# Performance work log

Hardware: AMD Instinct MI355X
Metric: run time of the kernel (lower is better)

Reference implementation:

```python
import jax, jax.numpy as jnp
import numpy as np

T, N, E = 12, 20000, 320000
FIN, H, G, C = 128, 256, 256, 10


def setup_inputs() -> dict:
    key = jax.random.key(0)
    ks = jax.random.split(key, 14)
    x = jax.random.normal(ks[0], (T, N, FIN), dtype=jnp.float32)
    edge_index = jax.random.randint(ks[1], (T, 2, E), 0, N)
    edge_attr = jax.random.uniform(ks[2], (T, E), dtype=jnp.float32)

    def lin(k, fan_in, shape):
        return jax.random.normal(k, shape, dtype=jnp.float32) / np.sqrt(fan_in).astype(np.float32)

    return {
        "x": x,
        "edge_index": edge_index,
        "edge_attr": edge_attr,
        "W1": lin(ks[3], FIN, (FIN, H)),
        "b1": jnp.zeros((H,), jnp.float32),
        "W2": lin(ks[4], H, (H, H)),
        "b2": jnp.zeros((H,), jnp.float32),
        "Wih": lin(ks[5], H, (3 * G, H)),
        "Whh": lin(ks[6], G, (3 * G, G)),
        "bih": jnp.zeros((3 * G,), jnp.float32),
        "bhh": jnp.zeros((3 * G,), jnp.float32),
        "Wc": lin(ks[7], G, (G, C)),
        "bc": jnp.zeros((C,), jnp.float32),
    }


def _gcn_conv(h, row, col, w, W, b):
    # PyG GCNConv: h' = D^{-1/2} (A + I) D^{-1/2} (h W) + b, with edge weights w
    h = h @ W  # [N, H]
    deg = jax.ops.segment_sum(w, col, num_segments=N) + 1.0  # self-loop weight 1
    dinv = jax.lax.rsqrt(deg)  # [N]
    norm = dinv[row] * w * dinv[col]  # [E]
    agg = jax.ops.segment_sum(norm[:, None] * h[row], col, num_segments=N)
    agg = agg + (dinv * dinv)[:, None] * h  # self-loop contribution
    return agg + b


def reference(x, edge_index, edge_attr, W1, b1, W2, b2, Wih, Whh, bih, bhh, Wc, bc):
    def snapshot(carry, inp):
        xs, ei, ea = inp
        row, col = ei[0], ei[1]
        h = jax.nn.relu(_gcn_conv(xs, row, col, ea, W1, b1))
        h = jax.nn.relu(_gcn_conv(h, row, col, ea, W2, b2))
        return carry, h.mean(axis=0)  # mean pool over nodes -> [H]

    _, embs = jax.lax.scan(snapshot, 0, (x, edge_index, edge_attr))  # [T, H]

    def gru_step(hprev, xt):
        gx = Wih @ xt + bih  # [3G]
        gh = Whh @ hprev + bhh
        r = jax.nn.sigmoid(gx[:G] + gh[:G])
        z = jax.nn.sigmoid(gx[G:2 * G] + gh[G:2 * G])
        n = jnp.tanh(gx[2 * G:] + r * gh[2 * G:])
        hnew = (1.0 - z) * n + z * hprev
        return hnew, None

    last_h, _ = jax.lax.scan(gru_step, jnp.zeros((G,), x.dtype), embs)
    out = last_h @ Wc + bc  # [C]
    return out[None, :]  # [1, num_classes]
```

## Files before the change

kernel.cpp:

```cpp
#include <hip/hip_runtime.h>
#include <hip/hip_fp16.h>
#include <math.h>

#define T_ 12
#define N_ 20000
#define E_ 320000
#define FIN_ 128
#define H_ 256
#define G_ 256
#define C_ 10
#define ECH 8
#define EPC (E_ / ECH)
#define NB 20
#define BNODES 1024
#define CAPF 20480

typedef __attribute__((ext_vector_type(8))) short bf16x8;
typedef __attribute__((ext_vector_type(4))) float f32x4;

static const size_t OFF_EMB   = 0;
static const size_t ZERO_BYTES= 12288;
static const size_t OFF_DINV  = 12288;
static const size_t OFF_CP    = 972288;
static const size_t OFF_PCNT  = 1932544;
static const size_t OFF_POFF  = 1940224;
static const size_t OFF_W1BT  = 1948288;
static const size_t OFF_W2BT  = 2013824;
static const size_t OFF_WIHT  = 2144896;
static const size_t OFF_WHHT  = 2931328;
static const size_t OFF_GX    = 3717760;
static const size_t OFF_EBIN  = 3754752;
static const size_t OFF_DEGP  = 3754752;
static const size_t OFF_CNT16 = 11434752;
static const size_t OFF_RA    = 34474752;
static const size_t PER_T_FULL= 10240000;

__device__ __forceinline__ float bf2f(unsigned short u) {
  return __uint_as_float(((unsigned int)u) << 16);
}
__device__ __forceinline__ unsigned short f2bf(float f) {
  unsigned int u = __float_as_uint(f);
  unsigned int r = (u + 0x7FFFu + ((u >> 16) & 1u)) >> 16;
  return (unsigned short)r;
}
__device__ __forceinline__ float bflo(unsigned int u) { return __uint_as_float(u << 16); }
__device__ __forceinline__ float bfhi(unsigned int u) { return __uint_as_float(u & 0xFFFF0000u); }
__device__ __forceinline__ unsigned int packbf(float lo, float hi) {
  return (unsigned int)f2bf(lo) | ((unsigned int)f2bf(hi) << 16);
}

__global__ __launch_bounds__(1024) void histp(const int* __restrict__ ei,
                                              const float* __restrict__ ea,
                                              float* __restrict__ degp,
                                              unsigned short* __restrict__ cnt16,
                                              unsigned int* __restrict__ pcnt) {
  __shared__ float degs[N_];
  __shared__ unsigned int cntp[N_ / 2];
  __shared__ unsigned int psum[NB];
  const int t = blockIdx.x, ech = blockIdx.y;
  const int tid = threadIdx.x;
  for (int i = tid; i < N_; i += 1024) degs[i] = 0.f;
  for (int i = tid; i < N_ / 2; i += 1024) cntp[i] = 0u;
  if (tid < NB) psum[tid] = 0u;
  __syncthreads();
  const int* col = ei + (size_t)t * 2 * E_ + E_ + ech * EPC;
  const float* wt = ea + (size_t)t * E_ + ech * EPC;
  for (int e = tid; e < EPC; e += 1024) {
    int c = col[e];
    atomicAdd(&degs[c], wt[e]);
    atomicAdd(&cntp[c >> 1], 1u << ((c & 1) * 16));
  }
  __syncthreads();
  float* dp = degp + ((size_t)t * ECH + ech) * N_;
  unsigned short* cp16 = cnt16 + ((size_t)t * ECH + ech) * N_;
  for (int i = tid; i < N_; i += 1024) {
    dp[i] = degs[i];
    cp16[i] = (unsigned short)((cntp[i >> 1] >> ((i & 1) * 16)) & 0xFFFFu);
  }
  for (int i = tid; i < N_ / 2; i += 1024) {
    unsigned int v = cntp[i];
    atomicAdd(&psum[i >> 9], (v & 0xFFFFu) + (v >> 16));
  }
  __syncthreads();
  if (tid < NB) pcnt[((size_t)t * ECH + ech) * NB + tid] = psum[tid];
}

__global__ __launch_bounds__(1024) void scanT(const unsigned short* __restrict__ cnt16,
                                              const float* __restrict__ degp,
                                              int* __restrict__ colptr,
                                              float* __restrict__ dinv) {
  const int t = blockIdx.x;
  __shared__ int s[1024];
  const int tid = threadIdx.x;
  int base = 0;
  for (int c0 = 0; c0 < N_; c0 += 1024) {
    int n = c0 + tid;
    int tot = 0;
    float dg = 0.f;
    if (n < N_) {
#pragma unroll
      for (int ch = 0; ch < ECH; ++ch) {
        tot += cnt16[((size_t)t * ECH + ch) * N_ + n];
        dg += degp[((size_t)t * ECH + ch) * N_ + n];
      }
    }
    s[tid] = tot;
    __syncthreads();
    for (int off = 1; off < 1024; off <<= 1) {
      int add = (tid >= off) ? s[tid - off] : 0;
      __syncthreads();
      s[tid] += add;
      __syncthreads();
    }
    if (n < N_) {
      colptr[t * (N_ + 1) + n] = base + s[tid] - tot;
      dinv[t * N_ + n] = rsqrtf(dg + 1.0f);
    }
    base += s[1023];
    __syncthreads();
  }
  if (tid == 0) colptr[t * (N_ + 1) + N_] = base;
}

__global__ void partS(const unsigned int* __restrict__ pcnt,
                      unsigned int* __restrict__ poff) {
  const int t = threadIdx.x;
  if (t >= T_) return;
  unsigned int run = 0;
  for (int b = 0; b < NB; ++b)
    for (int ech = 0; ech < ECH; ++ech) {
      poff[t * 168 + b * 8 + ech] = run;
      run += pcnt[((size_t)t * ECH + ech) * NB + b];
    }
  poff[t * 168 + 160] = run;
}

__global__ __launch_bounds__(512) void partW(const int* __restrict__ ei,
                                             const float* __restrict__ ea,
                                             const float* __restrict__ dinv,
                                             const unsigned int* __restrict__ poff,
                                             uint2* __restrict__ ebin) {
  __shared__ unsigned int cursor[NB];
  const int t = blockIdx.x, ech = blockIdx.y;
  const int tid = threadIdx.x;
  if (tid < NB) cursor[tid] = poff[t * 168 + tid * 8 + ech];
  __syncthreads();
  const int eoff = ech * EPC;
  const int* rowp = ei + (size_t)t * 2 * E_ + eoff;
  const int* colp = rowp + E_;
  const float* wt = ea + (size_t)t * E_ + eoff;
  const float* dv = dinv + (size_t)t * N_;
  uint2* eb = ebin + (size_t)t * E_;
  for (int e = tid; e < EPC; e += 512) {
    int c = colp[e], r = rowp[e];
    float nm = dv[r] * wt[e] * dv[c];
    unsigned int pos = atomicAdd(&cursor[c >> 10], 1u);
    uint2 rec;
    rec.x = (unsigned int)(c & 1023) | ((unsigned int)r << 16);
    rec.y = (unsigned int)__half_as_ushort(__float2half(nm));
    eb[pos] = rec;
  }
}

__global__ __launch_bounds__(512) void fillB2(uint2* __restrict__ ebin,
                                              const int* __restrict__ colptr) {
  __shared__ unsigned int data[CAPF];
  __shared__ unsigned int offp[BNODES];
  const int t = blockIdx.x, b = blockIdx.y;
  const int tid = threadIdx.x;
  const int nlo = b << 10;
  const int nnodes = (N_ - nlo < BNODES) ? (N_ - nlo) : BNODES;
  const int* cp = colptr + t * (N_ + 1);
  const int base = cp[nlo];
  const int bsize = cp[nlo + nnodes] - base;
  for (int i = tid; i < nnodes; i += 512) offp[i] = (unsigned int)(cp[nlo + i] - base);
  __syncthreads();
  uint2* eb = ebin + (size_t)t * E_ + base;
  for (int i = tid; i < bsize; i += 512) {
    uint2 rec = eb[i];
    unsigned int cl = rec.x & 0xFFFFu;
    unsigned int rec4 = (rec.x >> 16) | (rec.y << 16);
    unsigned int pos = atomicAdd(&offp[cl], 1u);
    if (pos < CAPF) data[pos] = rec4;
  }
  __syncthreads();
  const int lim = bsize < CAPF ? bsize : CAPF;
  for (int i = tid; i < lim; i += 512) {
    unsigned int rec4 = data[i];
    uint2 o;
    o.x = rec4 & 0xFFFFu;
    o.y = __float_as_uint(__half2float(__ushort_as_half((unsigned short)(rec4 >> 16))));
    eb[i] = o;
  }
}

__global__ __launch_bounds__(256) void prep_kernel(const float* __restrict__ W1,
                                                   const float* __restrict__ W2,
                                                   const float* __restrict__ Wih,
                                                   const float* __restrict__ Whh,
                                                   unsigned short* __restrict__ W1bT,
                                                   unsigned short* __restrict__ W2bT,
                                                   float* __restrict__ WihT,
                                                   float* __restrict__ WhhT) {
  int idx = blockIdx.x * 256 + threadIdx.x;
  if (idx < 32768) {
    int n = idx >> 7, k = idx & 127;
    W1bT[idx] = f2bf(W1[k * 256 + n]);
  } else if (idx < 98304) {
    int j = idx - 32768;
    int n = j >> 8, k = j & 255;
    W2bT[j] = f2bf(W2[k * 256 + n]);
  } else if (idx < 294912) {
    int j = idx - 98304;
    int k = j / 768, c = j - k * 768;
    WihT[j] = Wih[c * 256 + k];
  } else if (idx < 491520) {
    int j = idx - 294912;
    int k = j / 768, c = j - k * 768;
    WhhT[j] = Whh[c * 256 + k];
  }
}

__global__ __launch_bounds__(256) void castx_kernel(const float* __restrict__ x,
                                                    unsigned short* __restrict__ xb,
                                                    int t_base) {
  const int tl = blockIdx.y;
  const int t = t_base + tl;
  const size_t q = (size_t)blockIdx.x * 256 + threadIdx.x;
  float4 v = ((const float4*)x)[(size_t)t * (N_ * FIN_ / 4) + q];
  ushort4 o;
  o.x = f2bf(v.x); o.y = f2bf(v.y); o.z = f2bf(v.z); o.w = f2bf(v.w);
  ((ushort4*)xb)[(size_t)tl * (N_ * FIN_ / 4) + q] = o;
}

__device__ __forceinline__ void agg_decode(int nt, int t_base, int& t, int& tl, int& node) {
  int bid = blockIdx.x;
  int L = bid;
  if (nt > 1) {
    int chunk = (int)(gridDim.x >> 3);
    L = (bid & 7) * chunk + (bid >> 3);
  }
  tl = L / 5000;
  node = (L - tl * 5000) * 4 + ((int)threadIdx.x >> 6);
  t = t_base + nt > 1 ? t_base + tl : t_base + tl;
  t = t_base + tl;
}

__global__ __launch_bounds__(256) void agg128(const unsigned short* __restrict__ h,
                                              unsigned short* __restrict__ o,
                                              const uint2* __restrict__ erec2,
                                              const int* __restrict__ colptr,
                                              const float* __restrict__ dinv,
                                              int t_base, int nt) {
  int t, tl, node;
  agg_decode(nt, t_base, t, tl, node);
  const int q = ((int)threadIdx.x >> 4) & 3;
  const int l16 = threadIdx.x & 15;
  const int me = threadIdx.x & 63;
  const uint2* ert = erec2 + (size_t)t * E_;
  const int* cp = colptr + t * (N_ + 1);
  const unsigned short* ht = h + (size_t)tl * N_ * 128;
  float a0 = 0.f, a1 = 0.f, a2 = 0.f, a3 = 0.f, a4 = 0.f, a5 = 0.f, a6 = 0.f, a7 = 0.f;
  const int s0 = cp[node], s1 = cp[node + 1];
  const uint2 SAFE = {(unsigned int)node, 0u};
  {
    int i = s0 + q;
    uint2 r0 = (i < s1) ? ert[i] : SAFE;
    uint2 r1 = (i + 4 < s1) ? ert[i + 4] : SAFE;
    uint4 u0 = *(const uint4*)&ht[(size_t)r0.x * 128 + l16 * 8];
    for (int k = i; k < s1; k += 4) {
      uint2 r2 = (k + 8 < s1) ? ert[k + 8] : SAFE;
      uint4 u1 = *(const uint4*)&ht[(size_t)r1.x * 128 + l16 * 8];
      const float nm = __uint_as_float(r0.y);
      a0 = fmaf(nm, bflo(u0.x), a0); a1 = fmaf(nm, bfhi(u0.x), a1);
      a2 = fmaf(nm, bflo(u0.y), a2); a3 = fmaf(nm, bfhi(u0.y), a3);
      a4 = fmaf(nm, bflo(u0.z), a4); a5 = fmaf(nm, bfhi(u0.z), a5);
      a6 = fmaf(nm, bflo(u0.w), a6); a7 = fmaf(nm, bfhi(u0.w), a7);
      r0 = r1; r1 = r2; u0 = u1;
    }
  }
  if (q == 0) {
    const float di = dinv[(size_t)t * N_ + node];
    const float sw = di * di;
    uint4 us = *(const uint4*)&ht[(size_t)node * 128 + l16 * 8];
    a0 = fmaf(sw, bflo(us.x), a0); a1 = fmaf(sw, bfhi(us.x), a1);
    a2 = fmaf(sw, bflo(us.y), a2); a3 = fmaf(sw, bfhi(us.y), a3);
    a4 = fmaf(sw, bflo(us.z), a4); a5 = fmaf(sw, bfhi(us.z), a5);
    a6 = fmaf(sw, bflo(us.w), a6); a7 = fmaf(sw, bfhi(us.w), a7);
  }
  a0 += __shfl(a0, me | 16, 64); a1 += __shfl(a1, me | 16, 64);
  a2 += __shfl(a2, me | 16, 64); a3 += __shfl(a3, me | 16, 64);
  a4 += __shfl(a4, me | 16, 64); a5 += __shfl(a5, me | 16, 64);
  a6 += __shfl(a6, me | 16, 64); a7 += __shfl(a7, me | 16, 64);
  a0 += __shfl(a0, me | 32, 64); a1 += __shfl(a1, me | 32, 64);
  a2 += __shfl(a2, me | 32, 64); a3 += __shfl(a3, me | 32, 64);
  a4 += __shfl(a4, me | 32, 64); a5 += __shfl(a5, me | 32, 64);
  a6 += __shfl(a6, me | 32, 64); a7 += __shfl(a7, me | 32, 64);
  if (q == 0 && (me >> 4) == 0) {
    uint4 ov;
    ov.x = packbf(a0, a1); ov.y = packbf(a2, a3);
    ov.z = packbf(a4, a5); ov.w = packbf(a6, a7);
    *(uint4*)&o[((size_t)tl * N_ + node) * 128 + l16 * 8] = ov;
  }
}

__global__ __launch_bounds__(256) void agg256(const unsigned short* __restrict__ h,
                                              unsigned short* __restrict__ o,
                                              const uint2* __restrict__ erec2,
                                              const int* __restrict__ colptr,
                                              const float* __restrict__ dinv,
                                              int t_base, int nt) {
  int t, tl, node;
  agg_decode(nt, t_base, t, tl, node);
  const int hh = ((int)threadIdx.x >> 5) & 1;
  const int l32 = threadIdx.x & 31;
  const int me = threadIdx.x & 63;
  const uint2* ert = erec2 + (size_t)t * E_;
  const int* cp = colptr + t * (N_ + 1);
  const unsigned short* ht = h + (size_t)tl * N_ * 256;
  float a0 = 0.f, a1 = 0.f, a2 = 0.f, a3 = 0.f, a4 = 0.f, a5 = 0.f, a6 = 0.f, a7 = 0.f;
  const int s0 = cp[node], s1 = cp[node + 1];
  const uint2 SAFE = {(unsigned int)node, 0u};
  {
    int i = s0 + hh;
    uint2 r0 = (i < s1) ? ert[i] : SAFE;
    uint2 r1 = (i + 2 < s1) ? ert[i + 2] : SAFE;
    uint4 u0 = *(const uint4*)&ht[(size_t)r0.x * 256 + l32 * 8];
    for (int k = i; k < s1; k += 2) {
      uint2 r2 = (k + 4 < s1) ? ert[k + 4] : SAFE;
      uint4 u1 = *(const uint4*)&ht[(size_t)r1.x * 256 + l32 * 8];
      const float nm = __uint_as_float(r0.y);
      a0 = fmaf(nm, bflo(u0.x), a0); a1 = fmaf(nm, bfhi(u0.x), a1);
      a2 = fmaf(nm, bflo(u0.y), a2); a3 = fmaf(nm, bfhi(u0.y), a3);
      a4 = fmaf(nm, bflo(u0.z), a4); a5 = fmaf(nm, bfhi(u0.z), a5);
      a6 = fmaf(nm, bflo(u0.w), a6); a7 = fmaf(nm, bfhi(u0.w), a7);
      r0 = r1; r1 = r2; u0 = u1;
    }
  }
  if (hh == 0) {
    const float di = dinv[(size_t)t * N_ + node];
    const float sw = di * di;
    uint4 us = *(const uint4*)&ht[(size_t)node * 256 + l32 * 8];
    a0 = fmaf(sw, bflo(us.x), a0); a1 = fmaf(sw, bfhi(us.x), a1);
    a2 = fmaf(sw, bflo(us.y), a2); a3 = fmaf(sw, bfhi(us.y), a3);
    a4 = fmaf(sw, bflo(us.z), a4); a5 = fmaf(sw, bfhi(us.z), a5);
    a6 = fmaf(sw, bflo(us.w), a6); a7 = fmaf(sw, bfhi(us.w), a7);
  }
  a0 += __shfl(a0, me | 32, 64); a1 += __shfl(a1, me | 32, 64);
  a2 += __shfl(a2, me | 32, 64); a3 += __shfl(a3, me | 32, 64);
  a4 += __shfl(a4, me | 32, 64); a5 += __shfl(a5, me | 32, 64);
  a6 += __shfl(a6, me | 32, 64); a7 += __shfl(a7, me | 32, 64);
  if (hh == 0) {
    uint4 ov;
    ov.x = packbf(a0, a1); ov.y = packbf(a2, a3);
    ov.z = packbf(a4, a5); ov.w = packbf(a6, a7);
    *(uint4*)&o[((size_t)tl * N_ + node) * 256 + l32 * 8] = ov;
  }
}

template <int K, bool MEAN>
__global__ __launch_bounds__(256) void gemm_bf16(const unsigned short* __restrict__ A,
                                                 const unsigned short* __restrict__ BT,
                                                 const float* __restrict__ bias,
                                                 unsigned short* __restrict__ C,
                                                 float* __restrict__ embp,
                                                 int t_base) {
  constexpr int LD = K + 8;
  __shared__ unsigned short As[64 * LD];
  __shared__ float cs[128];
  const int tid = threadIdx.x;
  const int tl = blockIdx.z;
  const int bm = blockIdx.x * 64;
  const int bn = blockIdx.y * 128;
  const unsigned short* At = A + (size_t)tl * N_ * K;
  if (MEAN && tid < 128) cs[tid] = 0.f;
  {
    constexpr int CPR = K / 8;
    constexpr int CH = 64 * CPR / 256;
#pragma unroll
    for (int i = 0; i < CH; ++i) {
      int chunk = tid + i * 256;
      int r = chunk / CPR;
      int ck = (chunk - r * CPR) * 8;
      int row = bm + r;
      if (row >= N_) row = N_ - 1;
      *(bf16x8*)&As[r * LD + ck] = *(const bf16x8*)&At[(size_t)row * K + ck];
    }
  }
  __syncthreads();
  const int w = tid >> 6, l = tid & 63;
  const int l16 = l & 15, lk = l >> 4;
  const int rbase = (w >> 1) * 32;
  const int colbase = bn + (w & 1) * 64;
  f32x4 acc[2][4] = {};
  for (int ks = 0; ks < K; ks += 32) {
    bf16x8 a[2], b[4];
#pragma unroll
    for (int m = 0; m < 2; ++m)
      a[m] = *(const bf16x8*)&As[(rbase + m * 16 + l16) * LD + ks + lk * 8];
#pragma unroll
    for (int n = 0; n < 4; ++n)
      b[n] = *(const bf16x8*)&BT[(size_t)(colbase + n * 16 + l16) * K + ks + lk * 8];
#pragma unroll
    for (int m = 0; m < 2; ++m)
#pragma unroll
      for (int n = 0; n < 4; ++n)
        acc[m][n] = __builtin_amdgcn_mfma_f32_16x16x32_bf16(a[m], b[n], acc[m][n], 0, 0, 0);
  }
#pragma unroll
  for (int n = 0; n < 4; ++n) {
    int col = colbase + n * 16 + l16;
    float bv = bias[col];
    float psum = 0.f;
#pragma unroll
    for (int m = 0; m < 2; ++m) {
      int row0 = bm + rbase + m * 16 + lk * 4;
#pragma unroll
      for (int r = 0; r < 4; ++r) {
        int row = row0 + r;
        if (row < N_) {
          float v = fmaxf(acc[m][n][r] + bv, 0.f);
          if (MEAN) psum += v;
          else C[((size_t)tl * N_ + row) * 256 + col] = f2bf(v);
        }
      }
    }
    if (MEAN) atomicAdd(&cs[col - bn], psum);
  }
  if (MEAN) {
    __syncthreads();
    if (tid < 128)
      atomicAdd(&embp[(t_base + tl) * 256 + bn + tid], cs[tid] * (1.0f / N_));
  }
}

__global__ __launch_bounds__(768) void gx_kernel(const float* __restrict__ emb,
                                                 const float* __restrict__ WihT,
                                                 const float* __restrict__ bih,
                                                 float* __restrict__ GX) {
  const int t = blockIdx.x;
  const int tid = threadIdx.x;
  __shared__ float se[256];
  if (tid < 256) se[tid] = emb[t * 256 + tid];
  __syncthreads();
  float p0 = 0.f, p1 = 0.f, p2 = 0.f, p3 = 0.f;
#pragma unroll 8
  for (int k = 0; k < 256; k += 4) {
    p0 = fmaf(WihT[(size_t)(k + 0) * 768 + tid], se[k + 0], p0);
    p1 = fmaf(WihT[(size_t)(k + 1) * 768 + tid], se[k + 1], p1);
    p2 = fmaf(WihT[(size_t)(k + 2) * 768 + tid], se[k + 2], p2);
    p3 = fmaf(WihT[(size_t)(k + 3) * 768 + tid], se[k + 3], p3);
  }
  GX[t * 768 + tid] = (p0 + p1) + (p2 + p3) + bih[tid];
}

__global__ __launch_bounds__(768) void gru2_kernel(const float* __restrict__ GX,
                                                   const float* __restrict__ WhhT,
                                                   const float* __restrict__ bhh,
                                                   const float* __restrict__ Wc,
                                                   const float* __restrict__ bc,
                                                   float* __restrict__ out) {
  __shared__ float sh[256];
  __shared__ float sgh[768];
  const int tid = threadIdx.x;
  if (tid < 256) sh[tid] = 0.f;
  __syncthreads();
  for (int t = 0; t < T_; ++t) {
    float p0 = 0.f, p1 = 0.f, p2 = 0.f, p3 = 0.f;
#pragma unroll 8
    for (int k = 0; k < 256; k += 4) {
      p0 = fmaf(WhhT[(size_t)(k + 0) * 768 + tid], sh[k + 0], p0);
      p1 = fmaf(WhhT[(size_t)(k + 1) * 768 + tid], sh[k + 1], p1);
      p2 = fmaf(WhhT[(size_t)(k + 2) * 768 + tid], sh[k + 2], p2);
      p3 = fmaf(WhhT[(size_t)(k + 3) * 768 + tid], sh[k + 3], p3);
    }
    sgh[tid] = (p0 + p1) + (p2 + p3) + bhh[tid];
    __syncthreads();
    if (tid < 256) {
      const float* gx = &GX[t * 768];
      float r = 1.f / (1.f + __expf(-(gx[tid] + sgh[tid])));
      float z = 1.f / (1.f + __expf(-(gx[256 + tid] + sgh[256 + tid])));
      float n = tanhf(gx[512 + tid] + r * sgh[512 + tid]);
      sh[tid] = (1.f - z) * n + z * sh[tid];
    }
    __syncthreads();
  }
  const int wv = tid >> 6, lane = tid & 63;
  if (wv < C_) {
    float p = 0.f;
#pragma unroll
    for (int i = 0; i < 4; ++i) {
      int j = lane + 64 * i;
      p += sh[j] * Wc[(size_t)j * C_ + wv];
    }
    for (int off = 32; off > 0; off >>= 1) p += __shfl_down(p, off);
    if (lane == 0) out[wv] = p + bc[wv];
  }
}

extern "C" void kernel_launch(void* const* d_in, const int* in_sizes, int n_in,
                              void* d_out, int out_size, void* d_ws, size_t ws_size,
                              hipStream_t stream) {
  const float* x   = (const float*)d_in[0];
  const int*   ei  = (const int*)d_in[1];
  const float* ea  = (const float*)d_in[2];
  const float* W1  = (const float*)d_in[3];
  const float* b1  = (const float*)d_in[4];
  const float* W2  = (const float*)d_in[5];
  const float* b2  = (const float*)d_in[6];
  const float* Wih = (const float*)d_in[7];
  const float* Whh = (const float*)d_in[8];
  const float* bih = (const float*)d_in[9];
  const float* bhh = (const float*)d_in[10];
  const float* Wc  = (const float*)d_in[11];
  const float* bc  = (const float*)d_in[12];
  float* out = (float*)d_out;

  char* w = (char*)d_ws;
  float* emb   = (float*)(w + OFF_EMB);
  float* dinv  = (float*)(w + OFF_DINV);
  int*   cp    = (int*)(w + OFF_CP);
  unsigned int* pcnt = (unsigned int*)(w + OFF_PCNT);
  unsigned int* poff = (unsigned int*)(w + OFF_POFF);
  unsigned short* W1bT = (unsigned short*)(w + OFF_W1BT);
  unsigned short* W2bT = (unsigned short*)(w + OFF_W2BT);
  float* WihT  = (float*)(w + OFF_WIHT);
  float* WhhT  = (float*)(w + OFF_WHHT);
  float* GX    = (float*)(w + OFF_GX);
  float* degp  = (float*)(w + OFF_DEGP);
  unsigned short* cnt16 = (unsigned short*)(w + OFF_CNT16);
  uint2* ebin  = (uint2*)(w + OFF_EBIN);

  int NT = 1;
  if (ws_size > OFF_RA + 2 * PER_T_FULL) {
    size_t avail = ws_size - OFF_RA;
    size_t nt = avail / (2 * PER_T_FULL);
    NT = (int)(nt < 12 ? nt : 12);
    if (NT < 1) NT = 1;
  }
  unsigned short* regA = (unsigned short*)(w + OFF_RA);
  unsigned short* regB = (unsigned short*)(w + OFF_RA + (size_t)NT * PER_T_FULL);
  unsigned short* xbt  = regA;
  unsigned short* Q    = regA;
  unsigned short* P128 = regB;
  unsigned short* P2   = regB;

  hipMemsetAsync(d_ws, 0, ZERO_BYTES, stream);

  prep_kernel<<<1920, 256, 0, stream>>>(W1, W2, Wih, Whh, W1bT, W2bT, WihT, WhhT);

  dim3 te_grid(T_, ECH);
  histp<<<te_grid, 1024, 0, stream>>>(ei, ea, degp, cnt16, pcnt);
  scanT<<<T_, 1024, 0, stream>>>(cnt16, degp, cp, dinv);
  partS<<<1, 64, 0, stream>>>(pcnt, poff);
  partW<<<te_grid, 512, 0, stream>>>(ei, ea, dinv, poff, ebin);
  fillB2<<<dim3(T_, NB), 512, 0, stream>>>(ebin, cp);

  for (int t0 = 0; t0 < T_; t0 += NT) {
    const int nt = (T_ - t0) < NT ? (T_ - t0) : NT;
    castx_kernel<<<dim3(2500, nt), 256, 0, stream>>>(x, xbt, t0);
    agg128<<<nt * 5000, 256, 0, stream>>>(xbt, P128, (const uint2*)ebin, cp, dinv, t0, nt);
    gemm_bf16<FIN_, false><<<dim3(313, 2, nt), 256, 0, stream>>>(P128, W1bT, b1, Q, nullptr, t0);
    agg256<<<nt * 5000, 256, 0, stream>>>(Q, P2, (const uint2*)ebin, cp, dinv, t0, nt);
    gemm_bf16<H_, true><<<dim3(313, 2, nt), 256, 0, stream>>>(P2, W2bT, b2, nullptr, emb, t0);
  }
  gx_kernel<<<T_, 768, 0, stream>>>(emb, WihT, bih, GX);
  gru2_kernel<<<1, 768, 0, stream>>>(GX, WhhT, bhh, Wc, bc, out);
}
```

Baseline: 1.005 ms.

## Split aggregation feature columns into two passes and fold partition scan into scanT

Aggregation kernels now split each node's feature row into two column halves handled by separate blocks, doubling the grid. Within a block, four groups of lanes each take every fourth edge, so more edges are in flight per node and the reduction shuffles only across those groups. The one-thread-per-timestep partS kernel is replaced by a parallel shared-memory scan appended to scanT, removing one launch. The cost is that edge records and colptr are read twice per node, and agg128p uses narrower 8-byte gathers.

```diff
diff --git a/kernel.cpp b/kernel.cpp
--- a/kernel.cpp
+++ b/kernel.cpp
@@ -88,7 +88,9 @@
 __global__ __launch_bounds__(1024) void scanT(const unsigned short* __restrict__ cnt16,
                                               const float* __restrict__ degp,
                                               int* __restrict__ colptr,
-                                              float* __restrict__ dinv) {
+                                              float* __restrict__ dinv,
+                                              const unsigned int* __restrict__ pcnt,
+                                              unsigned int* __restrict__ poff) {
   const int t = blockIdx.x;
   __shared__ int s[1024];
   const int tid = threadIdx.x;
@@ -120,19 +122,21 @@
     __syncthreads();
   }
   if (tid == 0) colptr[t * (N_ + 1) + N_] = base;
-}
-
-__global__ void partS(const unsigned int* __restrict__ pcnt,
-                      unsigned int* __restrict__ poff) {
-  const int t = threadIdx.x;
-  if (t >= T_) return;
-  unsigned int run = 0;
-  for (int b = 0; b < NB; ++b)
-    for (int ech = 0; ech < ECH; ++ech) {
-      poff[t * 168 + b * 8 + ech] = run;
-      run += pcnt[((size_t)t * ECH + ech) * NB + b];
-    }
-  poff[t * 168 + 160] = run;
+  __syncthreads();
+  int v = 0;
+  if (tid < 160) {
+    int b = tid >> 3, ech = tid & 7;
+    v = (int)pcnt[((size_t)t * ECH + ech) * NB + b];
+  }
+  s[tid] = (tid < 160) ? v : 0;
+  __syncthreads();
+  for (int off = 1; off < 256; off <<= 1) {
+    int add = (tid >= off) ? s[tid - off] : 0;
+    __syncthreads();
+    s[tid] += add;
+    __syncthreads();
+  }
+  if (tid < 160) poff[t * 168 + tid] = (unsigned int)(s[tid] - v);
 }
 
 __global__ __launch_bounds__(512) void partW(const int* __restrict__ ei,
@@ -233,44 +237,42 @@
   ((ushort4*)xb)[(size_t)tl * (N_ * FIN_ / 4) + q] = o;
 }
 
-__device__ __forceinline__ void agg_decode(int nt, int t_base, int& t, int& tl, int& node) {
+__global__ __launch_bounds__(256) void agg256p(const unsigned short* __restrict__ h,
+                                               unsigned short* __restrict__ o,
+                                               const uint2* __restrict__ erec2,
+                                               const int* __restrict__ colptr,
+                                               const float* __restrict__ dinv,
+                                               int t_base, int nt) {
   int bid = blockIdx.x;
   int L = bid;
-  if (nt > 1) {
+  {
     int chunk = (int)(gridDim.x >> 3);
     L = (bid & 7) * chunk + (bid >> 3);
   }
-  tl = L / 5000;
-  node = (L - tl * 5000) * 4 + ((int)threadIdx.x >> 6);
-  t = t_base + nt > 1 ? t_base + tl : t_base + tl;
-  t = t_base + tl;
-}
-
-__global__ __launch_bounds__(256) void agg128(const unsigned short* __restrict__ h,
-                                              unsigned short* __restrict__ o,
-                                              const uint2* __restrict__ erec2,
-                                              const int* __restrict__ colptr,
-                                              const float* __restrict__ dinv,
-                                              int t_base, int nt) {
-  int t, tl, node;
-  agg_decode(nt, t_base, t, tl, node);
-  const int q = ((int)threadIdx.x >> 4) & 3;
-  const int l16 = threadIdx.x & 15;
+  const int PT = 2 * 5000;
+  const int tl = L / PT;
+  int rem = L - tl * PT;
+  const int pass = rem / 5000;
+  const int nb = rem - pass * 5000;
+  const int node = nb * 4 + ((int)threadIdx.x >> 6);
+  const int t = t_base + tl;
   const int me = threadIdx.x & 63;
+  const int g = me >> 4;
+  const int j = me & 15;
   const uint2* ert = erec2 + (size_t)t * E_;
   const int* cp = colptr + t * (N_ + 1);
-  const unsigned short* ht = h + (size_t)tl * N_ * 128;
+  const unsigned short* ht = h + (size_t)tl * N_ * 256 + pass * 128 + j * 8;
   float a0 = 0.f, a1 = 0.f, a2 = 0.f, a3 = 0.f, a4 = 0.f, a5 = 0.f, a6 = 0.f, a7 = 0.f;
   const int s0 = cp[node], s1 = cp[node + 1];
   const uint2 SAFE = {(unsigned int)node, 0u};
   {
-    int i = s0 + q;
+    int i = s0 + g;
     uint2 r0 = (i < s1) ? ert[i] : SAFE;
     uint2 r1 = (i + 4 < s1) ? ert[i + 4] : SAFE;
-    uint4 u0 = *(const uint4*)&ht[(size_t)r0.x * 128 + l16 * 8];
+    uint4 u0 = *(const uint4*)&ht[(size_t)r0.x * 256];
     for (int k = i; k < s1; k += 4) {
       uint2 r2 = (k + 8 < s1) ? ert[k + 8] : SAFE;
-      uint4 u1 = *(const uint4*)&ht[(size_t)r1.x * 128 + l16 * 8];
+      uint4 u1 = *(const uint4*)&ht[(size_t)r1.x * 256];
       const float nm = __uint_as_float(r0.y);
       a0 = fmaf(nm, bflo(u0.x), a0); a1 = fmaf(nm, bfhi(u0.x), a1);
       a2 = fmaf(nm, bflo(u0.y), a2); a3 = fmaf(nm, bfhi(u0.y), a3);
@@ -279,82 +281,90 @@
       r0 = r1; r1 = r2; u0 = u1;
     }
   }
-  if (q == 0) {
+  if (g == 0) {
     const float di = dinv[(size_t)t * N_ + node];
     const float sw = di * di;
-    uint4 us = *(const uint4*)&ht[(size_t)node * 128 + l16 * 8];
+    uint4 us = *(const uint4*)&ht[(size_t)node * 256];
     a0 = fmaf(sw, bflo(us.x), a0); a1 = fmaf(sw, bfhi(us.x), a1);
     a2 = fmaf(sw, bflo(us.y), a2); a3 = fmaf(sw, bfhi(us.y), a3);
     a4 = fmaf(sw, bflo(us.z), a4); a5 = fmaf(sw, bfhi(us.z), a5);
     a6 = fmaf(sw, bflo(us.w), a6); a7 = fmaf(sw, bfhi(us.w), a7);
   }
-  a0 += __shfl(a0, me | 16, 64); a1 += __shfl(a1, me | 16, 64);
-  a2 += __shfl(a2, me | 16, 64); a3 += __shfl(a3, me | 16, 64);
-  a4 += __shfl(a4, me | 16, 64); a5 += __shfl(a5, me | 16, 64);
-  a6 += __shfl(a6, me | 16, 64); a7 += __shfl(a7, me | 16, 64);
-  a0 += __shfl(a0, me | 32, 64); a1 += __shfl(a1, me | 32, 64);
-  a2 += __shfl(a2, me | 32, 64); a3 += __shfl(a3, me | 32, 64);
-  a4 += __shfl(a4, me | 32, 64); a5 += __shfl(a5, me | 32, 64);
-  a6 += __shfl(a6, me | 32, 64); a7 += __shfl(a7, me | 32, 64);
-  if (q == 0 && (me >> 4) == 0) {
+#pragma unroll
+  for (int off = 16; off <= 32; off <<= 1) {
+    a0 += __shfl(a0, me ^ off, 64); a1 += __shfl(a1, me ^ off, 64);
+    a2 += __shfl(a2, me ^ off, 64); a3 += __shfl(a3, me ^ off, 64);
+    a4 += __shfl(a4, me ^ off, 64); a5 += __shfl(a5, me ^ off, 64);
+    a6 += __shfl(a6, me ^ off, 64); a7 += __shfl(a7, me ^ off, 64);
+  }
+  if (g == 0) {
     uint4 ov;
     ov.x = packbf(a0, a1); ov.y = packbf(a2, a3);
     ov.z = packbf(a4, a5); ov.w = packbf(a6, a7);
-    *(uint4*)&o[((size_t)tl * N_ + node) * 128 + l16 * 8] = ov;
-  }
-}
-
-__global__ __launch_bounds__(256) void agg256(const unsigned short* __restrict__ h,
-                                              unsigned short* __restrict__ o,
-                                              const uint2* __restrict__ erec2,
-                                              const int* __restrict__ colptr,
-                                              const float* __restrict__ dinv,
-                                              int t_base, int nt) {
-  int t, tl, node;
-  agg_decode(nt, t_base, t, tl, node);
-  const int hh = ((int)threadIdx.x >> 5) & 1;
-  const int l32 = threadIdx.x & 31;
+    unsigned short* ot = o + (size_t)tl * N_ * 256 + pass * 128 + j * 8;
+    *(uint4*)&ot[(size_t)node * 256] = ov;
+  }
+}
+
+__global__ __launch_bounds__(256) void agg128p(const unsigned short* __restrict__ h,
+                                               unsigned short* __restrict__ o,
+                                               const uint2* __restrict__ erec2,
+                                               const int* __restrict__ colptr,
+                                               const float* __restrict__ dinv,
+                                               int t_base, int nt) {
+  int bid = blockIdx.x;
+  int L = bid;
+  {
+    int chunk = (int)(gridDim.x >> 3);
+    L = (bid & 7) * chunk + (bid >> 3);
+  }
+  const int PT = 2 * 5000;
+  const int tl = L / PT;
+  int rem = L - tl * PT;
+  const int pass = rem / 5000;
+  const int nb = rem - pass * 5000;
+  const int node = nb * 4 + ((int)threadIdx.x >> 6);
+  const int t = t_base + tl;
   const int me = threadIdx.x & 63;
+  const int g = me >> 4;
+  const int j = me & 15;
   const uint2* ert = erec2 + (size_t)t * E_;
   const int* cp = colptr + t * (N_ + 1);
-  const unsigned short* ht = h + (size_t)tl * N_ * 256;
-  float a0 = 0.f, a1 = 0.f, a2 = 0.f, a3 = 0.f, a4 = 0.f, a5 = 0.f, a6 = 0.f, a7 = 0.f;
+  const unsigned short* ht = h + (size_t)tl * N_ * 128 + pass * 64 + j * 4;
+  float a0 = 0.f, a1 = 0.f, a2 = 0.f, a3 = 0.f;
   const int s0 = cp[node], s1 = cp[node + 1];
   const uint2 SAFE = {(unsigned int)node, 0u};
   {
-    int i = s0 + hh;
+    int i = s0 + g;
     uint2 r0 = (i < s1) ? ert[i] : SAFE;
-    uint2 r1 = (i + 2 < s1) ? ert[i + 2] : SAFE;
-    uint4 u0 = *(const uint4*)&ht[(size_t)r0.x * 256 + l32 * 8];
-    for (int k = i; k < s1; k += 2) {
-      uint2 r2 = (k + 4 < s1) ? ert[k + 4] : SAFE;
-      uint4 u1 = *(const uint4*)&ht[(size_t)r1.x * 256 + l32 * 8];
+    uint2 r1 = (i + 4 < s1) ? ert[i + 4] : SAFE;
+    uint2 u0 = *(const uint2*)&ht[(size_t)r0.x * 128];
+    for (int k = i; k < s1; k += 4) {
+      uint2 r2 = (k + 8 < s1) ? ert[k + 8] : SAFE;
+      uint2 u1 = *(const uint2*)&ht[(size_t)r1.x * 128];
       const float nm = __uint_as_float(r0.y);
       a0 = fmaf(nm, bflo(u0.x), a0); a1 = fmaf(nm, bfhi(u0.x), a1);
       a2 = fmaf(nm, bflo(u0.y), a2); a3 = fmaf(nm, bfhi(u0.y), a3);
-      a4 = fmaf(nm, bflo(u0.z), a4); a5 = fmaf(nm, bfhi(u0.z), a5);
-      a6 = fmaf(nm, bflo(u0.w), a6); a7 = fmaf(nm, bfhi(u0.w), a7);
       r0 = r1; r1 = r2; u0 = u1;
     }
   }
-  if (hh == 0) {
+  if (g == 0) {
     const float di = dinv[(size_t)t * N_ + node];
     const float sw = di * di;
-    uint4 us = *(const uint4*)&ht[(size_t)node * 256 + l32 * 8];
+    uint2 us = *(const uint2*)&ht[(size_t)node * 128];
     a0 = fmaf(sw, bflo(us.x), a0); a1 = fmaf(sw, bfhi(us.x), a1);
     a2 = fmaf(sw, bflo(us.y), a2); a3 = fmaf(sw, bfhi(us.y), a3);
-    a4 = fmaf(sw, bflo(us.z), a4); a5 = fmaf(sw, bfhi(us.z), a5);
-    a6 = fmaf(sw, bflo(us.w), a6); a7 = fmaf(sw, bfhi(us.w), a7);
-  }
-  a0 += __shfl(a0, me | 32, 64); a1 += __shfl(a1, me | 32, 64);
-  a2 += __shfl(a2, me | 32, 64); a3 += __shfl(a3, me | 32, 64);
-  a4 += __shfl(a4, me | 32, 64); a5 += __shfl(a5, me | 32, 64);
-  a6 += __shfl(a6, me | 32, 64); a7 += __shfl(a7, me | 32, 64);
-  if (hh == 0) {
-    uint4 ov;
+  }
+#pragma unroll
+  for (int off = 16; off <= 32; off <<= 1) {
+    a0 += __shfl(a0, me ^ off, 64); a1 += __shfl(a1, me ^ off, 64);
+    a2 += __shfl(a2, me ^ off, 64); a3 += __shfl(a3, me ^ off, 64);
+  }
+  if (g == 0) {
+    uint2 ov;
     ov.x = packbf(a0, a1); ov.y = packbf(a2, a3);
-    ov.z = packbf(a4, a5); ov.w = packbf(a6, a7);
-    *(uint4*)&o[((size_t)tl * N_ + node) * 256 + l32 * 8] = ov;
+    unsigned short* ot = o + (size_t)tl * N_ * 128 + pass * 64 + j * 4;
+    *(uint2*)&ot[(size_t)node * 128] = ov;
   }
 }
 
@@ -551,17 +561,16 @@
 
   dim3 te_grid(T_, ECH);
   histp<<<te_grid, 1024, 0, stream>>>(ei, ea, degp, cnt16, pcnt);
-  scanT<<<T_, 1024, 0, stream>>>(cnt16, degp, cp, dinv);
-  partS<<<1, 64, 0, stream>>>(pcnt, poff);
+  scanT<<<T_, 1024, 0, stream>>>(cnt16, degp, cp, dinv, pcnt, poff);
   partW<<<te_grid, 512, 0, stream>>>(ei, ea, dinv, poff, ebin);
   fillB2<<<dim3(T_, NB), 512, 0, stream>>>(ebin, cp);
 
   for (int t0 = 0; t0 < T_; t0 += NT) {
     const int nt = (T_ - t0) < NT ? (T_ - t0) : NT;
     castx_kernel<<<dim3(2500, nt), 256, 0, stream>>>(x, xbt, t0);
-    agg128<<<nt * 5000, 256, 0, stream>>>(xbt, P128, (const uint2*)ebin, cp, dinv, t0, nt);
+    agg128p<<<nt * 10000, 256, 0, stream>>>(xbt, P128, (const uint2*)ebin, cp, dinv, t0, nt);
     gemm_bf16<FIN_, false><<<dim3(313, 2, nt), 256, 0, stream>>>(P128, W1bT, b1, Q, nullptr, t0);
-    agg256<<<nt * 5000, 256, 0, stream>>>(Q, P2, (const uint2*)ebin, cp, dinv, t0, nt);
+    agg256p<<<nt * 10000, 256, 0, stream>>>(Q, P2, (const uint2*)ebin, cp, dinv, t0, nt);
     gemm_bf16<H_, true><<<dim3(313, 2, nt), 256, 0, stream>>>(P2, W2bT, b2, nullptr, emb, t0);
   }
   gx_kernel<<<T_, 768, 0, stream>>>(emb, WihT, bih, GX);
```

Measured after the change: 1.112 ms. 1.11x slower.
